# Kernel optimization log

Measured on AMD Instinct MI355X. Metric: run time of the kernel, lower is better.

Reference implementation:

```python
import jax, jax.numpy as jnp
import numpy as np

N_NODES = 100000
N_EDGES = 1600000
N_GRAPHS = 512
NUM_REL = 3


def setup_inputs() -> dict:
    key = jax.random.key(0)
    ks = jax.random.split(key, 16)
    shape_idx = jax.random.randint(ks[0], (N_NODES,), 0, 16)
    color_idx = jax.random.randint(ks[1], (N_NODES,), 0, 8)
    node_feats = jnp.stack([shape_idx, color_idx], axis=1)  # [N,2] int
    edge_index = jax.random.randint(ks[2], (2, N_EDGES), 0, N_NODES)
    edge_type = jax.random.randint(ks[3], (N_EDGES,), 0, NUM_REL)
    batch = jnp.sort(jax.random.randint(ks[4], (N_NODES,), 0, N_GRAPHS))
    s = lambda k, sh: jax.random.normal(k, sh, dtype=jnp.float32) * 0.05
    return {
        'node_feats': node_feats,
        'edge_index': edge_index,
        'edge_type': edge_type,
        'batch': batch,
        'shape_emb': s(ks[5], (16, 8)),
        'color_emb': s(ks[6], (8, 8)),
        'pre_w': s(ks[7], (16, 32)),
        'pre_b': jnp.zeros((32,), jnp.float32),
        'root1': s(ks[8], (32, 64)),
        'rel1': s(ks[9], (NUM_REL, 32, 64)),
        'bias1': jnp.zeros((64,), jnp.float32),
        'root2': s(ks[10], (64, 64)),
        'rel2': s(ks[11], (NUM_REL, 64, 64)),
        'bias2': jnp.zeros((64,), jnp.float32),
        'cls_w': s(ks[12], (64, 10)),
        'cls_b': jnp.zeros((10,), jnp.float32),
    }


def rgcn_conv(x, edge_index, edge_type, root, rel_w, bias):
    # PyG RGCNConv: out_i = x_i @ root + sum_r mean_{j in N_r(i)} x_j @ W_r + bias
    src, dst = edge_index[0], edge_index[1]
    out = x @ root + bias
    xs = x[src]  # [E, in] gathered source features
    for r in range(NUM_REL):
        m = (edge_type == r).astype(x.dtype)  # [E]
        msg = (xs @ rel_w[r]) * m[:, None]  # [E, out]
        agg = jax.ops.segment_sum(msg, dst, num_segments=N_NODES)
        cnt = jax.ops.segment_sum(m, dst, num_segments=N_NODES)
        out = out + agg / jnp.maximum(cnt, 1.0)[:, None]
    return out


def reference(node_feats, edge_index, edge_type, batch, shape_emb, color_emb,
              pre_w, pre_b, root1, rel1, bias1, root2, rel2, bias2, cls_w, cls_b):
    x = jnp.concatenate([shape_emb[node_feats[:, 0]], color_emb[node_feats[:, 1]]], axis=1)  # [N,16]
    x = jax.nn.relu(x @ pre_w + pre_b)  # [N,32]
    x = jax.nn.relu(rgcn_conv(x, edge_index, edge_type, root1, rel1, bias1))  # [N,64]
    x = jax.nn.relu(rgcn_conv(x, edge_index, edge_type, root2, rel2, bias2))  # [N,64]
    # global_mean_pool over graph ids
    s = jax.ops.segment_sum(x, batch, num_segments=N_GRAPHS)
    c = jax.ops.segment_sum(jnp.ones((x.shape[0],), x.dtype), batch, num_segments=N_GRAPHS)
    pooled = s / jnp.maximum(c, 1.0)[:, None]  # [G,64]
    return pooled @ cls_w + cls_b  # [G,num_classes]
```

## Files before the change

### kernel.cpp

```cpp
#include <hip/hip_runtime.h>

#define NN 100000
#define NE 1600000
#define NG 512

#define BSH 9
#define NB 196
#define EPB 8192
#define NAB ((NE + EPB - 1) / EPB)
#define CAP 9216

__global__ __launch_bounds__(256) void k_embed(
    const int* __restrict__ nf, const float* __restrict__ semb,
    const float* __restrict__ cemb, const float* __restrict__ pw,
    const float* __restrict__ pb, float* __restrict__ x1)
{
  int gid = blockIdx.x * 256 + threadIdx.x;
  bool valid = gid < NN;
  int i = valid ? gid : NN - 1;
  int sf = nf[2 * i], cf = nf[2 * i + 1];
  float x0[16];
#pragma unroll
  for (int k = 0; k < 8; ++k) x0[k] = semb[sf * 8 + k];
#pragma unroll
  for (int k = 0; k < 8; ++k) x0[8 + k] = cemb[cf * 8 + k];
  float acc[32];
#pragma unroll
  for (int j = 0; j < 32; ++j) acc[j] = pb[j];
#pragma unroll
  for (int k = 0; k < 16; ++k) {
    float xv = x0[k];
#pragma unroll
    for (int j = 0; j < 32; ++j) acc[j] += xv * pw[k * 32 + j];
  }
  if (valid) {
    float4* o = (float4*)(x1 + (size_t)i * 32);
#pragma unroll
    for (int j4 = 0; j4 < 8; ++j4) {
      float4 v;
      v.x = fmaxf(acc[4 * j4 + 0], 0.f);
      v.y = fmaxf(acc[4 * j4 + 1], 0.f);
      v.z = fmaxf(acc[4 * j4 + 2], 0.f);
      v.w = fmaxf(acc[4 * j4 + 3], 0.f);
      o[j4] = v;
    }
  }
}


__global__ __launch_bounds__(256) void kA_count(
    const int* __restrict__ ei, int* __restrict__ bkt_cnt)
{
  __shared__ int lh[NB];
  for (int b = threadIdx.x; b < NB; b += 256) lh[b] = 0;
  __syncthreads();
  int base = blockIdx.x * EPB;
#pragma unroll
  for (int i = 0; i < EPB / 256; ++i) {
    int e = base + i * 256 + threadIdx.x;
    if (e < NE) atomicAdd(&lh[ei[NE + e] >> BSH], 1);
  }
  __syncthreads();
  for (int b = threadIdx.x; b < NB; b += 256)
    if (lh[b]) atomicAdd(&bkt_cnt[b], lh[b]);
}

__global__ __launch_bounds__(256) void kA_scan(
    const int* __restrict__ bkt_cnt, int* __restrict__ bkt_base,
    int* __restrict__ bkt_cur)
{
  __shared__ int sm[2][256];
  int t = threadIdx.x;
  int v = (t < NB) ? bkt_cnt[t] : 0;
  sm[0][t] = v;
  __syncthreads();
  int cur = 0;
#pragma unroll
  for (int off = 1; off < 256; off <<= 1) {
    int add = (t >= off) ? sm[cur][t - off] : 0;
    sm[cur ^ 1][t] = sm[cur][t] + add;
    __syncthreads();
    cur ^= 1;
  }
  if (t < NB) {
    int ex = sm[cur][t] - v;
    bkt_base[t] = ex;
    bkt_cur[t] = ex;
  }
  if (t == 0) bkt_base[NB] = NE;
}

__global__ __launch_bounds__(256) void kA_scatter(
    const int* __restrict__ ei, const int* __restrict__ et,
    int* __restrict__ bkt_cur, int* __restrict__ binned)
{
  __shared__ int packA[EPB];
  __shared__ unsigned char bktA[EPB];
  __shared__ int lh[NB], grun[NB], lcur[NB];
  for (int b = threadIdx.x; b < NB; b += 256) { lh[b] = 0; lcur[b] = 0; }
  __syncthreads();
  int base = blockIdx.x * EPB;
#pragma unroll
  for (int i = 0; i < EPB / 256; ++i) {
    int p = i * 256 + threadIdx.x;
    int e = base + p;
    if (e < NE) {
      int src = ei[e], dst = ei[NE + e], ty = et[e];
      int b = dst >> BSH;
      packA[p] = src | (ty << 17) | ((dst & 511) << 19);
      bktA[p] = (unsigned char)b;
      atomicAdd(&lh[b], 1);
    } else {
      bktA[p] = 255;
    }
  }
  __syncthreads();
  for (int b = threadIdx.x; b < NB; b += 256)
    grun[b] = lh[b] ? atomicAdd(&bkt_cur[b], lh[b]) : 0;
  __syncthreads();
#pragma unroll
  for (int i = 0; i < EPB / 256; ++i) {
    int p = i * 256 + threadIdx.x;
    int b = bktA[p];
    if (b != 255) {
      int off = atomicAdd(&lcur[b], 1);
      binned[grun[b] + off] = packA[p];
    }
  }
}

__global__ __launch_bounds__(512) void kB_build(
    const int* __restrict__ bkt_base, const int* __restrict__ binned,
    int* __restrict__ rs, int* __restrict__ ep)
{
  __shared__ int stage[CAP];
  __shared__ int ldeg[512], lrs[512], lcur[512];
  __shared__ int sm[2][512];
  int b = blockIdx.x;
  int t = threadIdx.x;
  int p0 = bkt_base[b], p1 = bkt_base[b + 1];
  int cnt = p1 - p0;
  int nodes0 = b << BSH;
  int nnodes = NN - nodes0 < 512 ? NN - nodes0 : 512;
  ldeg[t] = 0;
  lcur[t] = 0;
  __syncthreads();
  for (int p = t; p < cnt; p += 512) {
    int pk = binned[p0 + p];
    if (p < CAP) stage[p] = pk;
    atomicAdd(&ldeg[(pk >> 19) & 511], 1);
  }
  __syncthreads();
  sm[0][t] = ldeg[t];
  __syncthreads();
  int cur = 0;
#pragma unroll
  for (int off = 1; off < 512; off <<= 1) {
    int add = (t >= off) ? sm[cur][t - off] : 0;
    sm[cur ^ 1][t] = sm[cur][t] + add;
    __syncthreads();
    cur ^= 1;
  }
  lrs[t] = p0 + sm[cur][t] - ldeg[t];
  if (t < nnodes) rs[nodes0 + t] = lrs[t];
  if (b == NB - 1 && t == 0) rs[NN] = NE;
  __syncthreads();
  for (int p = t; p < cnt; p += 512) {
    int pk = (p < CAP) ? stage[p] : binned[p0 + p];
    int dl = (pk >> 19) & 511;
    int off = atomicAdd(&lcur[dl], 1);
    ep[lrs[dl] + off] = pk & 0x7FFFF;
  }
}

template <int IN>
__global__ __launch_bounds__(256) void k_agg(
    const float* __restrict__ x, const int* __restrict__ rs,
    const int* __restrict__ ep, float* __restrict__ h)
{
  constexpr int DPW = 64 / IN;
  int tid = threadIdx.x;
  int wid = (blockIdx.x * 256 + tid) >> 6;
  int lane = tid & 63;
  int k = lane & (IN - 1);
  int half = lane >> (IN == 64 ? 6 : 5);
  int d = wid * DPW + half;
  if (d >= NN) return;
  int p0 = rs[d], p1 = rs[d + 1];
  float a0 = 0.f, a1 = 0.f, a2 = 0.f;
  int c0 = 0, c1 = 0, c2 = 0;
  int p = p0;
  for (; p + 4 <= p1; p += 4) {
    int e0 = ep[p + 0];
    int e1 = ep[p + 1];
    int e2 = ep[p + 2];
    int e3 = ep[p + 3];
    float v0 = x[(size_t)(e0 & 0x1FFFF) * IN + k];
    float v1 = x[(size_t)(e1 & 0x1FFFF) * IN + k];
    float v2 = x[(size_t)(e2 & 0x1FFFF) * IN + k];
    float v3 = x[(size_t)(e3 & 0x1FFFF) * IN + k];
    int t0 = e0 >> 17, t1 = e1 >> 17, t2 = e2 >> 17, t3 = e3 >> 17;
    a0 += ((t0 == 0) ? v0 : 0.f) + ((t1 == 0) ? v1 : 0.f) +
          ((t2 == 0) ? v2 : 0.f) + ((t3 == 0) ? v3 : 0.f);
    a1 += ((t0 == 1) ? v0 : 0.f) + ((t1 == 1) ? v1 : 0.f) +
          ((t2 == 1) ? v2 : 0.f) + ((t3 == 1) ? v3 : 0.f);
    a2 += ((t0 == 2) ? v0 : 0.f) + ((t1 == 2) ? v1 : 0.f) +
          ((t2 == 2) ? v2 : 0.f) + ((t3 == 2) ? v3 : 0.f);
    c0 += (t0 == 0) + (t1 == 0) + (t2 == 0) + (t3 == 0);
    c1 += (t0 == 1) + (t1 == 1) + (t2 == 1) + (t3 == 1);
    c2 += (t0 == 2) + (t1 == 2) + (t2 == 2) + (t3 == 2);
  }
  for (; p < p1; ++p) {
    int e = ep[p];
    float v = x[(size_t)(e & 0x1FFFF) * IN + k];
    int t = e >> 17;
    a0 += (t == 0) ? v : 0.f;
    a1 += (t == 1) ? v : 0.f;
    a2 += (t == 2) ? v : 0.f;
    c0 += (t == 0);
    c1 += (t == 1);
    c2 += (t == 2);
  }
  float* hd = h + (size_t)d * 3 * IN;
  hd[0 * IN + k] = a0 / (float)(c0 > 0 ? c0 : 1);
  hd[1 * IN + k] = a1 / (float)(c1 > 0 ? c1 : 1);
  hd[2 * IN + k] = a2 / (float)(c2 > 0 ? c2 : 1);
}

template <int IN>
__global__ __launch_bounds__(512) void k_mat(
    const float* __restrict__ x, const float* __restrict__ h,
    const float* __restrict__ root, const float* __restrict__ rel,
    const float* __restrict__ bias, float* __restrict__ y)
{
  __shared__ float smem[3 * IN][65];
  const int tid = threadIdx.x;
  const int node0 = blockIdx.x * 64;
  const int n = tid & 63;
  const int j0 = __builtin_amdgcn_readfirstlane((tid >> 6) * 8);

  constexpr int F4 = IN / 4;
  constexpr int NPF = (64 * F4) / 512;

  for (int idx = tid; idx < 64 * F4; idx += 512) {
    int nn = idx / F4, c4 = idx % F4;
    int node = node0 + nn;
    float4 v = make_float4(0.f, 0.f, 0.f, 0.f);
    if (node < NN) v = *(const float4*)(x + (size_t)node * IN + c4 * 4);
    smem[c4 * 4 + 0][nn] = v.x;
    smem[c4 * 4 + 1][nn] = v.y;
    smem[c4 * 4 + 2][nn] = v.z;
    smem[c4 * 4 + 3][nn] = v.w;
  }
#pragma unroll
  for (int r = 0; r < 2; ++r) {
    for (int idx = tid; idx < 64 * F4; idx += 512) {
      int nn = idx / F4, c4 = idx % F4;
      int node = node0 + nn;
      float4 v = make_float4(0.f, 0.f, 0.f, 0.f);
      if (node < NN) v = *(const float4*)(h + ((size_t)node * 3 + r) * IN + c4 * 4);
      smem[(1 + r) * IN + c4 * 4 + 0][nn] = v.x;
      smem[(1 + r) * IN + c4 * 4 + 1][nn] = v.y;
      smem[(1 + r) * IN + c4 * 4 + 2][nn] = v.z;
      smem[(1 + r) * IN + c4 * 4 + 3][nn] = v.w;
    }
  }
  __syncthreads();

  float4 pf[NPF];
#pragma unroll
  for (int u = 0; u < NPF; ++u) {
    int idx = u * 512 + tid;
    int nn = idx / F4, c4 = idx % F4;
    int node = node0 + nn;
    pf[u] = make_float4(0.f, 0.f, 0.f, 0.f);
    if (node < NN) pf[u] = *(const float4*)(h + ((size_t)node * 3 + 2) * IN + c4 * 4);
  }

  float acc[8];
#pragma unroll
  for (int j = 0; j < 8; ++j) acc[j] = bias[j0 + j];

  auto mm = [&](const float* __restrict__ W, int row0) {
#pragma unroll 4
    for (int k = 0; k < IN; ++k) {
      float sk = smem[row0 + k][n];
      const float* w = W + (size_t)k * 64 + j0;
#pragma unroll
      for (int j = 0; j < 8; ++j) acc[j] = fmaf(sk, w[j], acc[j]);
    }
  };

  mm(root, 0);
  mm(rel, IN);
  mm(rel + (size_t)IN * 64, 2 * IN);
  __syncthreads();

#pragma unroll
  for (int u = 0; u < NPF; ++u) {
    int idx = u * 512 + tid;
    int nn = idx / F4, c4 = idx % F4;
    smem[c4 * 4 + 0][nn] = pf[u].x;
    smem[c4 * 4 + 1][nn] = pf[u].y;
    smem[c4 * 4 + 2][nn] = pf[u].z;
    smem[c4 * 4 + 3][nn] = pf[u].w;
  }
  __syncthreads();
  mm(rel + (size_t)2 * IN * 64, 0);

  int node = node0 + n;
  if (node < NN) {
    float4* o = (float4*)(y + (size_t)node * 64 + j0);
    float4 v;
    v.x = fmaxf(acc[0], 0.f);
    v.y = fmaxf(acc[1], 0.f);
    v.z = fmaxf(acc[2], 0.f);
    v.w = fmaxf(acc[3], 0.f);
    o[0] = v;
    v.x = fmaxf(acc[4], 0.f);
    v.y = fmaxf(acc[5], 0.f);
    v.z = fmaxf(acc[6], 0.f);
    v.w = fmaxf(acc[7], 0.f);
    o[1] = v;
  }
}

__global__ __launch_bounds__(256) void k_pool(
    const float* __restrict__ x3, const int* __restrict__ batch,
    float* __restrict__ pooled, float* __restrict__ gcnt)
{
  int gwave = (blockIdx.x * 256 + threadIdx.x) >> 6;
  int lane = threadIdx.x & 63;
  int n0 = gwave * 64;
  if (n0 >= NN) return;
  int n1 = n0 + 64 < NN ? n0 + 64 : NN;
  int gcur = batch[n0];
  float acc = 0.f;
  int run = 0;
  for (int n = n0; n < n1; ++n) {
    int g = batch[n];
    if (g != gcur) {
      atomicAdd(&pooled[gcur * 64 + lane], acc);
      if (lane == 0) atomicAdd(&gcnt[gcur], (float)run);
      acc = 0.f; run = 0; gcur = g;
    }
    acc += x3[(size_t)n * 64 + lane];
    ++run;
  }
  atomicAdd(&pooled[gcur * 64 + lane], acc);
  if (lane == 0) atomicAdd(&gcnt[gcur], (float)run);
}

__global__ __launch_bounds__(256) void k_cls(
    const float* __restrict__ pooled, const float* __restrict__ gcnt,
    const float* __restrict__ cw, const float* __restrict__ cb, float* __restrict__ out)
{
  int t = blockIdx.x * 256 + threadIdx.x;
  if (t >= NG * 10) return;
  int g = t / 10, c = t % 10;
  float cf = fmaxf(gcnt[g], 1.f);
  float acc = cb[c];
#pragma unroll 8
  for (int k = 0; k < 64; ++k)
    acc += (pooled[g * 64 + k] / cf) * cw[k * 10 + c];
  out[t] = acc;
}

extern "C" void kernel_launch(void* const* d_in, const int* in_sizes, int n_in,
                              void* d_out, int out_size, void* d_ws, size_t ws_size,
                              hipStream_t stream)
{
  const int* nf = (const int*)d_in[0];
  const int* ei = (const int*)d_in[1];
  const int* et = (const int*)d_in[2];
  const int* batch = (const int*)d_in[3];
  const float* semb = (const float*)d_in[4];
  const float* cemb = (const float*)d_in[5];
  const float* pw = (const float*)d_in[6];
  const float* pb = (const float*)d_in[7];
  const float* root1 = (const float*)d_in[8];
  const float* rel1 = (const float*)d_in[9];
  const float* bias1 = (const float*)d_in[10];
  const float* root2 = (const float*)d_in[11];
  const float* rel2 = (const float*)d_in[12];
  const float* bias2 = (const float*)d_in[13];
  const float* cw = (const float*)d_in[14];
  const float* cb = (const float*)d_in[15];
  float* out = (float*)d_out;

  char* ws = (char*)d_ws;
  size_t off = 0;
  auto alloc = [&](size_t bytes) {
    char* p = ws + off;
    off += (bytes + 255) & ~(size_t)255;
    return p;
  };
  int* bkt_cnt = (int*)alloc((size_t)NB * 4);
  int* bkt_base = (int*)alloc((size_t)(NB + 1) * 4);
  int* bkt_cur = (int*)alloc((size_t)NB * 4);
  int* rs = (int*)alloc((size_t)(NN + 1) * 4);
  int* ep = (int*)alloc((size_t)NE * 4);
  float* xA = (float*)alloc((size_t)NN * 64 * 4);
  float* xB = (float*)alloc((size_t)NN * 64 * 4);
  float* h = (float*)alloc((size_t)3 * NN * 64 * 4);
  float* pooled = (float*)alloc((size_t)NG * 64 * 4);
  float* gcnt = (float*)alloc((size_t)NG * 4);
  int* binned = (int*)h;
  (void)ws_size; (void)in_sizes; (void)n_in; (void)out_size;

  hipMemsetAsync(bkt_cnt, 0, (size_t)NB * 4, stream);
  k_embed<<<(NN + 255) / 256, 256, 0, stream>>>(nf, semb, cemb, pw, pb, xB);

  kA_count<<<NAB, 256, 0, stream>>>(ei, bkt_cnt);
  kA_scan<<<1, 256, 0, stream>>>(bkt_cnt, bkt_base, bkt_cur);
  kA_scatter<<<NAB, 256, 0, stream>>>(ei, et, bkt_cur, binned);
  kB_build<<<NB, 512, 0, stream>>>(bkt_base, binned, rs, ep);

  int matgrid = (NN + 63) / 64;

  k_agg<32><<<(NN / 2 + 3) / 4 + 1, 256, 0, stream>>>(xB, rs, ep, h);
  k_mat<32><<<matgrid, 512, 0, stream>>>(xB, h, root1, rel1, bias1, xA);
  k_agg<64><<<(NN + 3) / 4, 256, 0, stream>>>(xA, rs, ep, h);
  k_mat<64><<<matgrid, 512, 0, stream>>>(xA, h, root2, rel2, bias2, xB);

  hipMemsetAsync(pooled, 0, (size_t)NG * 64 * 4, stream);
  hipMemsetAsync(gcnt, 0, (size_t)NG * 4, stream);
  int nwaves = (NN + 63) / 64;
  k_pool<<<(nwaves + 3) / 4, 256, 0, stream>>>(xB, batch, pooled, gcnt);
  k_cls<<<(NG * 10 + 255) / 256, 256, 0, stream>>>(pooled, gcnt, cw, cb, out);
}
```

Measured before the change: 325.4 us.

## Sort CSR edges by (destination, relation) to drop per-edge type masking in aggregation

The CSR build now keys edges by destination node and relation type, so each node gets three contiguous segments with separate row starts (rs3). The aggregation kernel walks each relation segment with a single accumulator, and degree counts come from segment lengths. This removes the per-edge type compares and selects and the three masked accumulators. In exchange the build kernel uses three times more shared-memory counters and the row-start array is three times larger.

```diff
diff --git a/kernel.cpp b/kernel.cpp
--- a/kernel.cpp
+++ b/kernel.cpp
@@ -131,10 +131,10 @@
 
 __global__ __launch_bounds__(512) void kB_build(
     const int* __restrict__ bkt_base, const int* __restrict__ binned,
-    int* __restrict__ rs, int* __restrict__ ep)
+    int* __restrict__ rs3, int* __restrict__ ep)
 {
   __shared__ int stage[CAP];
-  __shared__ int ldeg[512], lrs[512], lcur[512];
+  __shared__ int ldeg3[1536], lrs3[1536], lcur3[1536];
   __shared__ int sm[2][512];
   int b = blockIdx.x;
   int t = threadIdx.x;
@@ -142,16 +142,19 @@
   int cnt = p1 - p0;
   int nodes0 = b << BSH;
   int nnodes = NN - nodes0 < 512 ? NN - nodes0 : 512;
-  ldeg[t] = 0;
-  lcur[t] = 0;
+  ldeg3[t] = 0; ldeg3[t + 512] = 0; ldeg3[t + 1024] = 0;
+  lcur3[t] = 0; lcur3[t + 512] = 0; lcur3[t + 1024] = 0;
   __syncthreads();
   for (int p = t; p < cnt; p += 512) {
     int pk = binned[p0 + p];
     if (p < CAP) stage[p] = pk;
-    atomicAdd(&ldeg[(pk >> 19) & 511], 1);
-  }
-  __syncthreads();
-  sm[0][t] = ldeg[t];
+    int key = ((pk >> 19) & 511) * 3 + ((pk >> 17) & 3);
+    atomicAdd(&ldeg3[key], 1);
+  }
+  __syncthreads();
+  int s0 = ldeg3[3 * t], s1 = ldeg3[3 * t + 1], s2 = ldeg3[3 * t + 2];
+  int tot = s0 + s1 + s2;
+  sm[0][t] = tot;
   __syncthreads();
   int cur = 0;
 #pragma unroll
@@ -161,21 +164,30 @@
     __syncthreads();
     cur ^= 1;
   }
-  lrs[t] = p0 + sm[cur][t] - ldeg[t];
-  if (t < nnodes) rs[nodes0 + t] = lrs[t];
-  if (b == NB - 1 && t == 0) rs[NN] = NE;
+  int ex = sm[cur][t] - tot;
+  int r0 = p0 + ex, r1 = r0 + s0, r2 = r1 + s1;
+  lrs3[3 * t] = r0;
+  lrs3[3 * t + 1] = r1;
+  lrs3[3 * t + 2] = r2;
+  if (t < nnodes) {
+    size_t base3 = (size_t)(nodes0 + t) * 3;
+    rs3[base3 + 0] = r0;
+    rs3[base3 + 1] = r1;
+    rs3[base3 + 2] = r2;
+  }
+  if (b == NB - 1 && t == 0) rs3[(size_t)NN * 3] = NE;
   __syncthreads();
   for (int p = t; p < cnt; p += 512) {
     int pk = (p < CAP) ? stage[p] : binned[p0 + p];
-    int dl = (pk >> 19) & 511;
-    int off = atomicAdd(&lcur[dl], 1);
-    ep[lrs[dl] + off] = pk & 0x7FFFF;
+    int key = ((pk >> 19) & 511) * 3 + ((pk >> 17) & 3);
+    int off = atomicAdd(&lcur3[key], 1);
+    ep[lrs3[key] + off] = pk & 0x1FFFF;
   }
 }
 
 template <int IN>
 __global__ __launch_bounds__(256) void k_agg(
-    const float* __restrict__ x, const int* __restrict__ rs,
+    const float* __restrict__ x, const int* __restrict__ rs3,
     const int* __restrict__ ep, float* __restrict__ h)
 {
   constexpr int DPW = 64 / IN;
@@ -186,45 +198,32 @@
   int half = lane >> (IN == 64 ? 6 : 5);
   int d = wid * DPW + half;
   if (d >= NN) return;
-  int p0 = rs[d], p1 = rs[d + 1];
-  float a0 = 0.f, a1 = 0.f, a2 = 0.f;
-  int c0 = 0, c1 = 0, c2 = 0;
-  int p = p0;
-  for (; p + 4 <= p1; p += 4) {
-    int e0 = ep[p + 0];
-    int e1 = ep[p + 1];
-    int e2 = ep[p + 2];
-    int e3 = ep[p + 3];
-    float v0 = x[(size_t)(e0 & 0x1FFFF) * IN + k];
-    float v1 = x[(size_t)(e1 & 0x1FFFF) * IN + k];
-    float v2 = x[(size_t)(e2 & 0x1FFFF) * IN + k];
-    float v3 = x[(size_t)(e3 & 0x1FFFF) * IN + k];
-    int t0 = e0 >> 17, t1 = e1 >> 17, t2 = e2 >> 17, t3 = e3 >> 17;
-    a0 += ((t0 == 0) ? v0 : 0.f) + ((t1 == 0) ? v1 : 0.f) +
-          ((t2 == 0) ? v2 : 0.f) + ((t3 == 0) ? v3 : 0.f);
-    a1 += ((t0 == 1) ? v0 : 0.f) + ((t1 == 1) ? v1 : 0.f) +
-          ((t2 == 1) ? v2 : 0.f) + ((t3 == 1) ? v3 : 0.f);
-    a2 += ((t0 == 2) ? v0 : 0.f) + ((t1 == 2) ? v1 : 0.f) +
-          ((t2 == 2) ? v2 : 0.f) + ((t3 == 2) ? v3 : 0.f);
-    c0 += (t0 == 0) + (t1 == 0) + (t2 == 0) + (t3 == 0);
-    c1 += (t0 == 1) + (t1 == 1) + (t2 == 1) + (t3 == 1);
-    c2 += (t0 == 2) + (t1 == 2) + (t2 == 2) + (t3 == 2);
-  }
-  for (; p < p1; ++p) {
-    int e = ep[p];
-    float v = x[(size_t)(e & 0x1FFFF) * IN + k];
-    int t = e >> 17;
-    a0 += (t == 0) ? v : 0.f;
-    a1 += (t == 1) ? v : 0.f;
-    a2 += (t == 2) ? v : 0.f;
-    c0 += (t == 0);
-    c1 += (t == 1);
-    c2 += (t == 2);
-  }
+  int q0 = rs3[3 * d + 0];
+  int q1 = rs3[3 * d + 1];
+  int q2 = rs3[3 * d + 2];
+  int q3 = rs3[3 * d + 3];
   float* hd = h + (size_t)d * 3 * IN;
-  hd[0 * IN + k] = a0 / (float)(c0 > 0 ? c0 : 1);
-  hd[1 * IN + k] = a1 / (float)(c1 > 0 ? c1 : 1);
-  hd[2 * IN + k] = a2 / (float)(c2 > 0 ? c2 : 1);
+#pragma unroll
+  for (int r = 0; r < 3; ++r) {
+    int pA = (r == 0) ? q0 : (r == 1) ? q1 : q2;
+    int pB = (r == 0) ? q1 : (r == 1) ? q2 : q3;
+    float a = 0.f;
+    int p = pA;
+    for (; p + 4 <= pB; p += 4) {
+      int e0 = ep[p + 0];
+      int e1 = ep[p + 1];
+      int e2 = ep[p + 2];
+      int e3 = ep[p + 3];
+      float v0 = x[(size_t)e0 * IN + k];
+      float v1 = x[(size_t)e1 * IN + k];
+      float v2 = x[(size_t)e2 * IN + k];
+      float v3 = x[(size_t)e3 * IN + k];
+      a += (v0 + v1) + (v2 + v3);
+    }
+    for (; p < pB; ++p) a += x[(size_t)ep[p] * IN + k];
+    int c = pB - pA;
+    hd[r * IN + k] = a / (float)(c > 0 ? c : 1);
+  }
 }
 
 template <int IN>
@@ -398,7 +397,7 @@
   int* bkt_cnt = (int*)alloc((size_t)NB * 4);
   int* bkt_base = (int*)alloc((size_t)(NB + 1) * 4);
   int* bkt_cur = (int*)alloc((size_t)NB * 4);
-  int* rs = (int*)alloc((size_t)(NN + 1) * 4);
+  int* rs3 = (int*)alloc(((size_t)NN * 3 + 1) * 4);
   int* ep = (int*)alloc((size_t)NE * 4);
   float* xA = (float*)alloc((size_t)NN * 64 * 4);
   float* xB = (float*)alloc((size_t)NN * 64 * 4);
@@ -414,13 +413,13 @@
   kA_count<<<NAB, 256, 0, stream>>>(ei, bkt_cnt);
   kA_scan<<<1, 256, 0, stream>>>(bkt_cnt, bkt_base, bkt_cur);
   kA_scatter<<<NAB, 256, 0, stream>>>(ei, et, bkt_cur, binned);
-  kB_build<<<NB, 512, 0, stream>>>(bkt_base, binned, rs, ep);
+  kB_build<<<NB, 512, 0, stream>>>(bkt_base, binned, rs3, ep);
 
   int matgrid = (NN + 63) / 64;
 
-  k_agg<32><<<(NN / 2 + 3) / 4 + 1, 256, 0, stream>>>(xB, rs, ep, h);
+  k_agg<32><<<(NN / 2 + 3) / 4 + 1, 256, 0, stream>>>(xB, rs3, ep, h);
   k_mat<32><<<matgrid, 512, 0, stream>>>(xB, h, root1, rel1, bias1, xA);
-  k_agg<64><<<(NN + 3) / 4, 256, 0, stream>>>(xA, rs, ep, h);
+  k_agg<64><<<(NN + 3) / 4, 256, 0, stream>>>(xA, rs3, ep, h);
   k_mat<64><<<matgrid, 512, 0, stream>>>(xA, h, root2, rel2, bias2, xB);
 
   hipMemsetAsync(pooled, 0, (size_t)NG * 64 * 4, stream);
```

Result: slower. 349.0 us (+7.3%).
